# Performance work log

Measured on AMD Instinct MI355X. Metric: run time of the kernel, lower is better.

## Reference

```python
import jax, jax.numpy as jnp
import numpy as np

# ---- structural constants (mirror e3nn SO3.tensor_productRs bookkeeping) ----
MUL = 2                      # multiplicity of every irrep in Rs_in / Rs_out
LS = [0, 1, 2]               # irrep orders present in Rs_in and Rs_out
L_MAX = 2                    # spherical-harmonics cutoff -> Y_dim = 9
N_BASIS, HIDDEN = 64, 64     # radial model sizes
R_MAX, GAMMA = 3.5, 4.0      # gaussian radial basis params


def _filter_paths():
    """One entry (l_filter) per (mul_out, mul_in, l_in, l_out, l_f) path."""
    paths = []
    for l_in in LS:
        for l_out in LS:
            for lf in range(abs(l_in - l_out), min(l_in + l_out, L_MAX) + 1):
                paths.extend([lf] * (MUL * MUL))  # mul_in * mul_out copies
    return paths  # len == n_path == 60


def _build_mix_matrices():
    """rf_mix[K, n_path]: broadcast each radial path weight over its 2l+1 components.
    ylm_mix[K, 9]: select Y_{l,m} for each filter component. Both 0/1, block sparse."""
    paths = _filter_paths()
    n_path = len(paths)
    K = sum(2 * l + 1 for l in paths)          # 204
    y_off = {0: 0, 1: 1, 2: 4}                 # offset of l-block inside Y (dim 9)
    rf = np.zeros((K, n_path), dtype=np.float32)
    ylm = np.zeros((K, 9), dtype=np.float32)
    k = 0
    for p, l in enumerate(paths):
        for m in range(2 * l + 1):
            rf[k, p] = 1.0
            ylm[k, y_off[l] + m] = 1.0
            k += 1
    return rf, ylm, n_path, K


def _sh_l012(n):
    """Real spherical harmonics l=0..2 on unit vectors n[Z,3] -> Y[9, Z]."""
    x, y, z = n[:, 0], n[:, 1], n[:, 2]
    c0 = 0.28209479177387814   # 1/(2 sqrt(pi))
    c1 = 0.4886025119029199    # sqrt(3/(4 pi))
    c2a = 1.0925484305920792   # sqrt(15/(4 pi))
    c2b = 0.31539156525252005  # sqrt(5/(16 pi))
    c2c = 0.5462742152960396   # sqrt(15/(16 pi))
    one = jnp.ones_like(x)
    return jnp.stack([
        c0 * one,
        c1 * y, c1 * z, c1 * x,
        c2a * x * y, c2a * y * z, c2b * (3.0 * z * z - 1.0), c2a * x * z,
        c2c * (x * x - y * y),
    ], axis=0)


def setup_inputs() -> dict:
    key = jax.random.key(0)
    k_r, k_cg, k_w1, k_w2 = jax.random.split(key, 4)
    Z = 65536
    D = MUL * sum(2 * l + 1 for l in LS)       # 18 (dim_in == dim_out)
    rf_np, ylm_np, n_path, K = _build_mix_matrices()
    r = 2.0 * jax.random.normal(k_r, (Z, 3), dtype=jnp.float32)
    cg = jax.random.normal(k_cg, (K, D, D), dtype=jnp.float32) / np.sqrt(K)
    W1 = jax.random.normal(k_w1, (N_BASIS, HIDDEN), dtype=jnp.float32) / np.sqrt(N_BASIS)
    b1 = jnp.zeros((HIDDEN,), dtype=jnp.float32)
    W2 = jax.random.normal(k_w2, (HIDDEN, n_path), dtype=jnp.float32) / np.sqrt(HIDDEN)
    b2 = jnp.zeros((n_path,), dtype=jnp.float32)
    return {"r": r, "W1": W1, "b1": b1, "W2": W2, "b2": b2,
            "cg": cg, "rf_mix": jnp.asarray(rf_np), "ylm_mix": jnp.asarray(ylm_np)}


def reference(r, W1, b1, W2, b2, cg, rf_mix, ylm_mix):
    radii = jnp.linalg.norm(r, axis=1)                    # [Z]
    n = r / (radii[:, None] + 1e-12)                      # unit directions
    Y = _sh_l012(n)                                       # [9, Z]  (sh returns [m, ...])
    centers = jnp.linspace(0.0, R_MAX, N_BASIS, dtype=jnp.float32)
    B = jnp.exp(-GAMMA * (radii[:, None] - centers) ** 2) # gaussian radial basis [Z, 64]
    R = jax.nn.relu(B @ W1 + b1) @ W2 + b2                # RadialModel -> [Z, n_path]
    Rm = jnp.einsum('kp,zp->zk', rf_mix, R)               # 'ij,zj->zi'
    Ym = jnp.einsum('ky,yz->zk', ylm_mix, Y)              # 'ij,jz->zi'
    # 'kij,zk,zk->zij' : fuse the two per-point vectors, then one GEMM over k
    kernel = jnp.einsum('kij,zk->zij', cg, Rm * Ym)       # [Z, 18, 18]
    return kernel
```

## Files before the change

kernel.cpp:

```cpp
#include <hip/hip_runtime.h>

#define NPATH 60
#define KDIM  204
#define NIJ   324
#define NTIL  21
#define HID   64

typedef short bf16x8 __attribute__((ext_vector_type(8)));
typedef float f32x4  __attribute__((ext_vector_type(4)));

__device__ __align__(16) unsigned short g_w1s[4096];
__device__ __align__(16) unsigned short g_w2s[4096];
__device__ __align__(16) unsigned short g_cgs[75264];
__device__ unsigned int  g_pyk[112];

__device__ inline unsigned short f2bf(float f) {
    unsigned int u = __builtin_bit_cast(unsigned int, f);
    u += 0x7fffu + ((u >> 16) & 1u);
    return (unsigned short)(u >> 16);
}
__device__ inline float bf2f(unsigned short h) {
    unsigned int u = ((unsigned int)h) << 16;
    return __builtin_bit_cast(float, u);
}

__global__ void prep_kernel(const float* __restrict__ W1, const float* __restrict__ W2,
                            const float* __restrict__ cg, const float* __restrict__ rf,
                            const float* __restrict__ ylm)
{
    int idx = blockIdx.x * 256 + threadIdx.x;
    if (idx < 4096) {
        int e = idx & 7, ln = (idx >> 3) & 63, nt = (idx >> 9) & 3, kc = idx >> 11;
        int k = kc * 32 + (ln >> 4) * 8 + e;
        int n = nt * 16 + (ln & 15);
        g_w1s[idx] = f2bf(W1[k * HID + n]);
    } else if (idx < 8192) {
        int j = idx - 4096;
        int e = j & 7, ln = (j >> 3) & 63, nt = (j >> 9) & 3, kc = j >> 11;
        int k = kc * 32 + (ln >> 4) * 8 + e;
        int n = nt * 16 + (ln & 15);
        g_w2s[j] = f2bf(n < NPATH ? W2[k * NPATH + n] : 0.0f);
    } else if (idx < 8192 + 75264) {
        int j = idx - 8192;
        int e = j & 7, ln = (j >> 3) & 63;
        int nt = (j >> 9) % NTIL;
        int kc = j / (512 * NTIL);
        int k = kc * 32 + (ln >> 4) * 8 + e;
        int n = nt * 16 + (ln & 15);
        g_cgs[j] = f2bf((k < KDIM && n < NIJ) ? cg[k * NIJ + n] : 0.0f);
    } else if (idx < 8192 + 75264 + 112) {
        int j = idx - (8192 + 75264);
        int k0 = 2 * j, k1 = 2 * j + 1;
        unsigned p0 = 0, y0 = 0, p1 = 0, y1 = 0;
        if (k0 < KDIM) {
            for (int q = 0; q < NPATH; q++) if (rf[k0 * NPATH + q] != 0.0f) p0 = q;
            for (int q = 0; q < 9; q++)     if (ylm[k0 * 9 + q]   != 0.0f) y0 = q;
            for (int q = 0; q < NPATH; q++) if (rf[k1 * NPATH + q] != 0.0f) p1 = q;
            for (int q = 0; q < 9; q++)     if (ylm[k1 * 9 + q]   != 0.0f) y1 = q;
        }
        g_pyk[j] = p0 | (y0 << 8) | (p1 << 16) | (y1 << 24);
    }
}

struct __align__(16) WaveMem {
    union {
        unsigned short Hw[16][88];
        unsigned short Cw[16][224];
    } u;
    unsigned short Rw[16][61];
    float          Yw[16][9];
};

__global__ __launch_bounds__(256) void fused_kernel(
    const float* __restrict__ r, const float* __restrict__ b1,
    const float* __restrict__ b2, float* __restrict__ out)
{
    __shared__ WaveMem wm[4];
    __shared__ unsigned int pyw[112];

    const int tid  = threadIdx.x;
    const int wv   = tid >> 6;
    const int lane = tid & 63;
    const int quad = lane >> 4;
    const int l16  = lane & 15;
    const int z0   = blockIdx.x * 64;

    pyw[lane] = g_pyk[lane];
    if (lane < 48) pyw[64 + lane] = g_pyk[64 + lane];

    const int zloc = wv * 16 + l16;
    const int zg   = z0 + zloc;
    float x = r[zg * 3 + 0], y = r[zg * 3 + 1], zc = r[zg * 3 + 2];
    float rad = sqrtf(x * x + y * y + zc * zc);

    if (quad == 0) {
        float inv = 1.0f / (rad + 1e-12f);
        float nx = x * inv, ny = y * inv, nz = zc * inv;
        const float c0 = 0.28209479177387814f, c1 = 0.4886025119029199f;
        const float c2a = 1.0925484305920792f, c2b = 0.31539156525252005f, c2c = 0.5462742152960396f;
        wm[wv].Yw[l16][0] = c0;
        wm[wv].Yw[l16][1] = c1 * ny;
        wm[wv].Yw[l16][2] = c1 * nz;
        wm[wv].Yw[l16][3] = c1 * nx;
        wm[wv].Yw[l16][4] = c2a * nx * ny;
        wm[wv].Yw[l16][5] = c2a * ny * nz;
        wm[wv].Yw[l16][6] = c2b * (3.0f * nz * nz - 1.0f);
        wm[wv].Yw[l16][7] = c2a * nx * nz;
        wm[wv].Yw[l16][8] = c2c * (nx * nx - ny * ny);
    }

    union { bf16x8 v; unsigned int d[4]; } A0, A1;
    {
        const float step = 3.5f / 63.0f;
        const float NL2E = -5.770780163555852f;
        #pragma unroll
        for (int ii = 0; ii < 4; ii++) {
            int i0 = quad * 8 + 2 * ii;
            float d0 = rad - (float)i0 * step;
            float d1 = rad - (float)(i0 + 1) * step;
            A0.d[ii] = (unsigned)f2bf(__builtin_amdgcn_exp2f(d0 * d0 * NL2E))
                     | ((unsigned)f2bf(__builtin_amdgcn_exp2f(d1 * d1 * NL2E)) << 16);
            int i2 = 32 + i0;
            float e0 = rad - (float)i2 * step;
            float e1 = rad - (float)(i2 + 1) * step;
            A1.d[ii] = (unsigned)f2bf(__builtin_amdgcn_exp2f(e0 * e0 * NL2E))
                     | ((unsigned)f2bf(__builtin_amdgcn_exp2f(e1 * e1 * NL2E)) << 16);
        }
    }

    #pragma unroll
    for (int nt = 0; nt < 4; nt++) {
        bf16x8 bb0 = *(const bf16x8*)&g_w1s[((0 * 4 + nt) * 64 + lane) * 8];
        bf16x8 bb1 = *(const bf16x8*)&g_w1s[((1 * 4 + nt) * 64 + lane) * 8];
        f32x4 acc = {0.f, 0.f, 0.f, 0.f};
        acc = __builtin_amdgcn_mfma_f32_16x16x32_bf16(A0.v, bb0, acc, 0, 0, 0);
        acc = __builtin_amdgcn_mfma_f32_16x16x32_bf16(A1.v, bb1, acc, 0, 0, 0);
        int h = nt * 16 + l16;
        float bias = b1[h];
        #pragma unroll
        for (int rr = 0; rr < 4; rr++) {
            float v = acc[rr] + bias;
            v = v > 0.0f ? v : 0.0f;
            wm[wv].u.Hw[quad * 4 + rr][h] = f2bf(v);
        }
    }
    asm volatile("s_waitcnt lgkmcnt(0)" ::: "memory");
    __builtin_amdgcn_sched_barrier(0);

    {
        bf16x8 h0 = *(const bf16x8*)&wm[wv].u.Hw[l16][0 + quad * 8];
        bf16x8 h1 = *(const bf16x8*)&wm[wv].u.Hw[l16][32 + quad * 8];
        #pragma unroll
        for (int nt = 0; nt < 4; nt++) {
            bf16x8 bb0 = *(const bf16x8*)&g_w2s[((0 * 4 + nt) * 64 + lane) * 8];
            bf16x8 bb1 = *(const bf16x8*)&g_w2s[((1 * 4 + nt) * 64 + lane) * 8];
            f32x4 acc = {0.f, 0.f, 0.f, 0.f};
            acc = __builtin_amdgcn_mfma_f32_16x16x32_bf16(h0, bb0, acc, 0, 0, 0);
            acc = __builtin_amdgcn_mfma_f32_16x16x32_bf16(h1, bb1, acc, 0, 0, 0);
            int p = nt * 16 + l16;
            if (p < NPATH) {
                float bias = b2[p];
                #pragma unroll
                for (int rr = 0; rr < 4; rr++)
                    wm[wv].Rw[quad * 4 + rr][p] = f2bf(acc[rr] + bias);
            }
        }
    }
    asm volatile("s_waitcnt lgkmcnt(0)" ::: "memory");
    __builtin_amdgcn_sched_barrier(0);

    {
        const unsigned gkey = ((unsigned)((l16 >> 2) & 3)) << 2;
        unsigned int* crow = (unsigned int*)&wm[wv].u.Cw[l16][0];
        #pragma unroll
        for (int jj = 0; jj < 28; jj++) {
            int j = quad * 28 + jj;
            unsigned u = 0;
            if (2 * j < KDIM) {
                unsigned py = pyw[j];
                float cA = bf2f(wm[wv].Rw[l16][py & 255])          * wm[wv].Yw[l16][(py >> 8) & 255];
                float cB = bf2f(wm[wv].Rw[l16][(py >> 16) & 255])  * wm[wv].Yw[l16][py >> 24];
                u = (unsigned)f2bf(cA) | ((unsigned)f2bf(cB) << 16);
            }
            crow[j ^ gkey] = u;
        }
    }

    __syncthreads();

    const int ntb = wv * 5 + (wv > 0 ? 1 : 0);
    const int cnt = (wv == 0) ? 6 : 5;
    const unsigned bkey = ((unsigned)((l16 >> 2) & 3)) << 4;

    #pragma unroll
    for (int half = 0; half < 2; half++) {
        f32x4 acc[3][4];
        #pragma unroll
        for (int ii = 0; ii < 3; ii++)
            #pragma unroll
            for (int zt = 0; zt < 4; zt++)
                acc[ii][zt] = (f32x4){0.f, 0.f, 0.f, 0.f};

        #pragma unroll
        for (int kc = 0; kc < 7; kc++) {
            bf16x8 az[4];
            #pragma unroll
            for (int zt = 0; zt < 4; zt++) {
                unsigned boff = ((unsigned)(kc * 64 + quad * 16)) ^ bkey;
                az[zt] = *(const bf16x8*)((const char*)&wm[zt].u.Cw[l16][0] + boff);
            }
            bf16x8 bg[3];
            #pragma unroll
            for (int ii = 0; ii < 3; ii++) {
                int nt = ntb + half * 3 + ii; if (nt > NTIL - 1) nt = NTIL - 1;
                bg[ii] = *(const bf16x8*)&g_cgs[((kc * NTIL + nt) * 64 + lane) * 8];
            }
            #pragma unroll
            for (int ii = 0; ii < 3; ii++) {
                if (half * 3 + ii < cnt) {
                    #pragma unroll
                    for (int zt = 0; zt < 4; zt++)
                        acc[ii][zt] = __builtin_amdgcn_mfma_f32_16x16x32_bf16(az[zt], bg[ii], acc[ii][zt], 0, 0, 0);
                }
            }
        }

        #pragma unroll
        for (int ii = 0; ii < 3; ii++) {
            if (half * 3 + ii < cnt) {
                int col = (ntb + half * 3 + ii) * 16 + l16;
                if (col < NIJ) {
                    #pragma unroll
                    for (int zt = 0; zt < 4; zt++) {
                        #pragma unroll
                        for (int rr = 0; rr < 4; rr++)
                            out[(z0 + zt * 16 + quad * 4 + rr) * NIJ + col] = acc[ii][zt][rr];
                    }
                }
            }
        }
    }
}

extern "C" void kernel_launch(void* const* d_in, const int* in_sizes, int n_in,
                              void* d_out, int out_size, void* d_ws, size_t ws_size,
                              hipStream_t stream) {
    const float* r   = (const float*)d_in[0];
    const float* W1  = (const float*)d_in[1];
    const float* b1  = (const float*)d_in[2];
    const float* W2  = (const float*)d_in[3];
    const float* b2  = (const float*)d_in[4];
    const float* cg  = (const float*)d_in[5];
    const float* rf  = (const float*)d_in[6];
    const float* ylm = (const float*)d_in[7];
    float* out = (float*)d_out;

    const int Z = in_sizes[0] / 3;

    prep_kernel<<<327, 256, 0, stream>>>(W1, W2, cg, rf, ylm);
    fused_kernel<<<Z / 64, 256, 0, stream>>>(r, b1, b2, out);
}
```

Before: 138.2 us.

## Build CG-GEMM A fragments in registers and give each wave its own rows

Each wave now computes the full 324-column output for its own 16 points instead of splitting column tiles across waves for all 64 points. The Rm*Ym operand is built directly in registers as MFMA A fragments, which removes the shared-memory C staging buffer, the pyw copy and the block-wide __syncthreads. In exchange, each CG B fragment is now loaded once per 16 points instead of being reused across 4 point tiles, so global/L1 traffic on the CG table rises about fourfold. Padded k entries now compute nonzero products, but they are multiplied by zero-padded CG rows, so the output is unchanged.

```diff
diff --git a/kernel.cpp b/kernel.cpp
--- a/kernel.cpp
+++ b/kernel.cpp
@@ -63,10 +63,7 @@
 }
 
 struct __align__(16) WaveMem {
-    union {
-        unsigned short Hw[16][88];
-        unsigned short Cw[16][224];
-    } u;
+    unsigned short Hw[16][88];
     unsigned short Rw[16][61];
     float          Yw[16][9];
 };
@@ -76,7 +73,6 @@
     const float* __restrict__ b2, float* __restrict__ out)
 {
     __shared__ WaveMem wm[4];
-    __shared__ unsigned int pyw[112];
 
     const int tid  = threadIdx.x;
     const int wv   = tid >> 6;
@@ -84,12 +80,9 @@
     const int quad = lane >> 4;
     const int l16  = lane & 15;
     const int z0   = blockIdx.x * 64;
-
-    pyw[lane] = g_pyk[lane];
-    if (lane < 48) pyw[64 + lane] = g_pyk[64 + lane];
-
-    const int zloc = wv * 16 + l16;
-    const int zg   = z0 + zloc;
+    WaveMem& W = wm[wv];
+
+    const int zg = z0 + wv * 16 + l16;
     float x = r[zg * 3 + 0], y = r[zg * 3 + 1], zc = r[zg * 3 + 2];
     float rad = sqrtf(x * x + y * y + zc * zc);
 
@@ -98,18 +91,19 @@
         float nx = x * inv, ny = y * inv, nz = zc * inv;
         const float c0 = 0.28209479177387814f, c1 = 0.4886025119029199f;
         const float c2a = 1.0925484305920792f, c2b = 0.31539156525252005f, c2c = 0.5462742152960396f;
-        wm[wv].Yw[l16][0] = c0;
-        wm[wv].Yw[l16][1] = c1 * ny;
-        wm[wv].Yw[l16][2] = c1 * nz;
-        wm[wv].Yw[l16][3] = c1 * nx;
-        wm[wv].Yw[l16][4] = c2a * nx * ny;
-        wm[wv].Yw[l16][5] = c2a * ny * nz;
-        wm[wv].Yw[l16][6] = c2b * (3.0f * nz * nz - 1.0f);
-        wm[wv].Yw[l16][7] = c2a * nx * nz;
-        wm[wv].Yw[l16][8] = c2c * (nx * nx - ny * ny);
-    }
-
-    union { bf16x8 v; unsigned int d[4]; } A0, A1;
+        W.Yw[l16][0] = c0;
+        W.Yw[l16][1] = c1 * ny;
+        W.Yw[l16][2] = c1 * nz;
+        W.Yw[l16][3] = c1 * nx;
+        W.Yw[l16][4] = c2a * nx * ny;
+        W.Yw[l16][5] = c2a * ny * nz;
+        W.Yw[l16][6] = c2b * (3.0f * nz * nz - 1.0f);
+        W.Yw[l16][7] = c2a * nx * nz;
+        W.Yw[l16][8] = c2c * (nx * nx - ny * ny);
+    }
+
+    union frag { bf16x8 v; unsigned int d[4]; };
+    frag A0, A1;
     {
         const float step = 3.5f / 63.0f;
         const float NL2E = -5.770780163555852f;
@@ -141,15 +135,15 @@
         for (int rr = 0; rr < 4; rr++) {
             float v = acc[rr] + bias;
             v = v > 0.0f ? v : 0.0f;
-            wm[wv].u.Hw[quad * 4 + rr][h] = f2bf(v);
+            W.Hw[quad * 4 + rr][h] = f2bf(v);
         }
     }
     asm volatile("s_waitcnt lgkmcnt(0)" ::: "memory");
     __builtin_amdgcn_sched_barrier(0);
 
     {
-        bf16x8 h0 = *(const bf16x8*)&wm[wv].u.Hw[l16][0 + quad * 8];
-        bf16x8 h1 = *(const bf16x8*)&wm[wv].u.Hw[l16][32 + quad * 8];
+        bf16x8 h0 = *(const bf16x8*)&W.Hw[l16][0 + quad * 8];
+        bf16x8 h1 = *(const bf16x8*)&W.Hw[l16][32 + quad * 8];
         #pragma unroll
         for (int nt = 0; nt < 4; nt++) {
             bf16x8 bb0 = *(const bf16x8*)&g_w2s[((0 * 4 + nt) * 64 + lane) * 8];
@@ -162,82 +156,39 @@
                 float bias = b2[p];
                 #pragma unroll
                 for (int rr = 0; rr < 4; rr++)
-                    wm[wv].Rw[quad * 4 + rr][p] = f2bf(acc[rr] + bias);
+                    W.Rw[quad * 4 + rr][p] = f2bf(acc[rr] + bias);
             }
         }
     }
     asm volatile("s_waitcnt lgkmcnt(0)" ::: "memory");
     __builtin_amdgcn_sched_barrier(0);
 
-    {
-        const unsigned gkey = ((unsigned)((l16 >> 2) & 3)) << 2;
-        unsigned int* crow = (unsigned int*)&wm[wv].u.Cw[l16][0];
-        #pragma unroll
-        for (int jj = 0; jj < 28; jj++) {
-            int j = quad * 28 + jj;
-            unsigned u = 0;
-            if (2 * j < KDIM) {
-                unsigned py = pyw[j];
-                float cA = bf2f(wm[wv].Rw[l16][py & 255])          * wm[wv].Yw[l16][(py >> 8) & 255];
-                float cB = bf2f(wm[wv].Rw[l16][(py >> 16) & 255])  * wm[wv].Yw[l16][py >> 24];
-                u = (unsigned)f2bf(cA) | ((unsigned)f2bf(cB) << 16);
-            }
-            crow[j ^ gkey] = u;
-        }
-    }
-
-    __syncthreads();
-
-    const int ntb = wv * 5 + (wv > 0 ? 1 : 0);
-    const int cnt = (wv == 0) ? 6 : 5;
-    const unsigned bkey = ((unsigned)((l16 >> 2) & 3)) << 4;
-
+    frag az[7];
     #pragma unroll
-    for (int half = 0; half < 2; half++) {
-        f32x4 acc[3][4];
-        #pragma unroll
-        for (int ii = 0; ii < 3; ii++)
+    for (int kc = 0; kc < 7; kc++) {
+        #pragma unroll
+        for (int ii = 0; ii < 4; ii++) {
+            unsigned py = g_pyk[kc * 16 + quad * 4 + ii];
+            float cA = bf2f(W.Rw[l16][py & 255])         * W.Yw[l16][(py >> 8) & 255];
+            float cB = bf2f(W.Rw[l16][(py >> 16) & 255]) * W.Yw[l16][py >> 24];
+            az[kc].d[ii] = (unsigned)f2bf(cA) | ((unsigned)f2bf(cB) << 16);
+        }
+    }
+
+    const int obase = (z0 + wv * 16 + quad * 4) * NIJ + l16;
+    #pragma unroll 3
+    for (int nt = 0; nt < NTIL; nt++) {
+        f32x4 acc = {0.f, 0.f, 0.f, 0.f};
+        #pragma unroll
+        for (int kc = 0; kc < 7; kc++) {
+            bf16x8 bg = *(const bf16x8*)&g_cgs[((kc * NTIL + nt) * 64 + lane) * 8];
+            acc = __builtin_amdgcn_mfma_f32_16x16x32_bf16(az[kc].v, bg, acc, 0, 0, 0);
+        }
+        int col = nt * 16 + l16;
+        if (col < NIJ) {
             #pragma unroll
-            for (int zt = 0; zt < 4; zt++)
-                acc[ii][zt] = (f32x4){0.f, 0.f, 0.f, 0.f};
-
-        #pragma unroll
-        for (int kc = 0; kc < 7; kc++) {
-            bf16x8 az[4];
-            #pragma unroll
-            for (int zt = 0; zt < 4; zt++) {
-                unsigned boff = ((unsigned)(kc * 64 + quad * 16)) ^ bkey;
-                az[zt] = *(const bf16x8*)((const char*)&wm[zt].u.Cw[l16][0] + boff);
-            }
-            bf16x8 bg[3];
-            #pragma unroll
-            for (int ii = 0; ii < 3; ii++) {
-                int nt = ntb + half * 3 + ii; if (nt > NTIL - 1) nt = NTIL - 1;
-                bg[ii] = *(const bf16x8*)&g_cgs[((kc * NTIL + nt) * 64 + lane) * 8];
-            }
-            #pragma unroll
-            for (int ii = 0; ii < 3; ii++) {
-                if (half * 3 + ii < cnt) {
-                    #pragma unroll
-                    for (int zt = 0; zt < 4; zt++)
-                        acc[ii][zt] = __builtin_amdgcn_mfma_f32_16x16x32_bf16(az[zt], bg[ii], acc[ii][zt], 0, 0, 0);
-                }
-            }
-        }
-
-        #pragma unroll
-        for (int ii = 0; ii < 3; ii++) {
-            if (half * 3 + ii < cnt) {
-                int col = (ntb + half * 3 + ii) * 16 + l16;
-                if (col < NIJ) {
-                    #pragma unroll
-                    for (int zt = 0; zt < 4; zt++) {
-                        #pragma unroll
-                        for (int rr = 0; rr < 4; rr++)
-                            out[(z0 + zt * 16 + quad * 4 + rr) * NIJ + col] = acc[ii][zt][rr];
-                    }
-                }
-            }
+            for (int rr = 0; rr < 4; rr++)
+                out[obase + rr * NIJ + nt * 16] = acc[rr];
         }
     }
 }
```

Measured after the change: 127.2 us. -7.9%, faster.
